# Kernel tuning notes

Hardware: AMD Instinct MI355X
Metric: run time of the kernel (lower is better)

Reference implementation:

```python
import jax, jax.numpy as jnp
import numpy as np

B, N, D = 16, 1024, 768
H = 12
HD = D // H           # 64
NUM_BUCKETS = 49      # iRPE 'product' buckets, shared across heads
SCALE = HD ** -0.5


def setup_inputs() -> dict:
    key = jax.random.key(0)
    k1, k2, k3, k4, k5, k6 = jax.random.split(key, 6)
    x = jax.random.normal(k1, (B, N, D), dtype=jnp.float32)
    qkv_w = jax.random.normal(k2, (3 * D, D), dtype=jnp.float32) * 0.02
    rpe_table = jax.random.normal(k3, (NUM_BUCKETS, HD), dtype=jnp.float32) * 0.02
    rp_bucket = jax.random.randint(k4, (N, N), 0, NUM_BUCKETS, dtype=jnp.int32)
    proj_w = jax.random.normal(k5, (D, D), dtype=jnp.float32) * 0.02
    proj_b = jax.random.normal(k6, (D,), dtype=jnp.float32) * 0.02
    return {"x": x, "qkv_w": qkv_w, "rpe_table": rpe_table,
            "rp_bucket": rp_bucket, "proj_w": proj_w, "proj_b": proj_b}


def reference(x, qkv_w, rpe_table, rp_bucket, proj_w, proj_b):
    b, n, d = x.shape
    # qkv projection (no bias), split into q,k,v of shape [B,H,N,HD]
    qkv = (x @ qkv_w.T).reshape(b, n, 3, H, HD)
    qkv = jnp.transpose(qkv, (2, 0, 3, 1, 4))
    q, k, v = qkv[0], qkv[1], qkv[2]
    q = q * SCALE
    # full attention scores [B,H,N,N]
    attn = jnp.einsum('bhid,bhjd->bhij', q, k)
    # iRPE contextual bias on keys: project q onto the bucket table, then
    # gather per relative-position bucket: bias[b,h,i,j] = (q @ W^T)[b,h,i,rp_bucket[i,j]]
    bias_all = jnp.einsum('bhid,cd->bhic', q, rpe_table)   # [B,H,N,num_buckets]
    bias = bias_all[:, :, jnp.arange(n)[:, None], rp_bucket]  # [B,H,N,N]
    attn = jax.nn.softmax(attn + bias, axis=-1)
    out = jnp.einsum('bhij,bhjd->bhid', attn, v)            # [B,H,N,HD]
    out = jnp.transpose(out, (0, 2, 1, 3)).reshape(b, n, d)
    return out @ proj_w.T + proj_b
```

## Files before the change

### kernel.cpp

```cpp
#include <hip/hip_runtime.h>

typedef short bf16x8 __attribute__((ext_vector_type(8)));
typedef float f32x4 __attribute__((ext_vector_type(4)));


__device__ __forceinline__ unsigned short f2bf(float f){
  unsigned u = __float_as_uint(f);
  u = (u + 0x7fffu + ((u >> 16) & 1u)) >> 16;
  return (unsigned short)u;
}
__device__ __forceinline__ float bf2f(unsigned short u){
  return __uint_as_float(((unsigned)u) << 16);
}
__device__ __forceinline__ f32x4 mfma16(bf16x8 a, bf16x8 b, f32x4 c){
  return __builtin_amdgcn_mfma_f32_16x16x32_bf16(a, b, c, 0, 0, 0);
}
__device__ __forceinline__ void gload_lds16(const void* g, void* l){
  __builtin_amdgcn_global_load_lds((__attribute__((address_space(1))) void*)(g),
                                   (__attribute__((address_space(3))) void*)(l), 16, 0, 0);
}

__global__ __launch_bounds__(256) void prep_kernel(
    const float* __restrict__ x, const float* __restrict__ qw,
    const float* __restrict__ pw, const int* __restrict__ rp,
    unsigned short* __restrict__ xb, unsigned short* __restrict__ wb,
    unsigned short* __restrict__ pwb, unsigned char* __restrict__ rp8){
  const int T1 = 3145728;
  const int T2 = T1 + 442368;
  const int T3 = T2 + 147456;
  const int T4 = T3 + 262144;
  for (int t = blockIdx.x * 256 + threadIdx.x; t < T4; t += gridDim.x * 256){
    if (t < T3){
      const float4* src; ushort4* dst; int off;
      if (t < T1){ src = (const float4*)x;  dst = (ushort4*)xb;  off = t; }
      else if (t < T2){ src = (const float4*)qw; dst = (ushort4*)wb;  off = t - T1; }
      else { src = (const float4*)pw; dst = (ushort4*)pwb; off = t - T2; }
      float4 v = src[off];
      ushort4 u;
      u.x = f2bf(v.x); u.y = f2bf(v.y); u.z = f2bf(v.z); u.w = f2bf(v.w);
      dst[off] = u;
    } else {
      int off = t - T3;
      int4 v = ((const int4*)rp)[off];
      uchar4 u;
      u.x = (unsigned char)v.x; u.y = (unsigned char)v.y;
      u.z = (unsigned char)v.z; u.w = (unsigned char)v.w;
      ((uchar4*)rp8)[off] = u;
    }
  }
}

__device__ __forceinline__ void gemm_core(
    const unsigned short* __restrict__ A, const unsigned short* __restrict__ Bm,
    int m0, int n0, int K, unsigned short* As, unsigned short* Bs,
    f32x4 (&acc)[4][4]){
  const int tid = threadIdx.x, lane = tid & 63, wave = tid >> 6;
  const int g = lane >> 4, r16 = lane & 15;
  const int wr = wave >> 1, wc = wave & 1;
  for (int k0 = 0; k0 < K; k0 += 32){
    __syncthreads();
    #pragma unroll
    for (int j = 0; j < 2; j++){
      int ci = j * 256 + tid;
      int row = ci >> 2, c = ci & 3;
      gload_lds16(A  + (size_t)(m0 + row) * K + k0 + c * 8,
                  (char*)As + (j * 256 + wave * 64) * 16);
      gload_lds16(Bm + (size_t)(n0 + row) * K + k0 + c * 8,
                  (char*)Bs + (j * 256 + wave * 64) * 16);
    }
    __syncthreads();
    bf16x8 a[4], b[4];
    #pragma unroll
    for (int mi = 0; mi < 4; mi++)
      a[mi] = *(const bf16x8*)((const char*)As + (wr * 64 + mi * 16 + r16) * 64 + g * 16);
    #pragma unroll
    for (int ni = 0; ni < 4; ni++)
      b[ni] = *(const bf16x8*)((const char*)Bs + (wc * 64 + ni * 16 + r16) * 64 + g * 16);
    #pragma unroll
    for (int mi = 0; mi < 4; mi++)
      #pragma unroll
      for (int ni = 0; ni < 4; ni++)
        acc[mi][ni] = mfma16(a[mi], b[ni], acc[mi][ni]);
  }
}

__global__ __launch_bounds__(256) void qkv_gemm(
    const unsigned short* __restrict__ xb, const unsigned short* __restrict__ wb,
    unsigned short* __restrict__ q_s, unsigned short* __restrict__ k_s,
    unsigned short* __restrict__ v_t){
  __shared__ __align__(16) unsigned short As[128 * 32];
  __shared__ __align__(16) unsigned short Bs[128 * 32];
  f32x4 acc[4][4];
  #pragma unroll
  for (int i = 0; i < 4; i++)
    #pragma unroll
    for (int j = 0; j < 4; j++){
      acc[i][j][0] = 0.f; acc[i][j][1] = 0.f; acc[i][j][2] = 0.f; acc[i][j][3] = 0.f;
    }
  const int m0 = blockIdx.y * 128, n0 = blockIdx.x * 128;
  gemm_core(xb, wb, m0, n0, 768, As, Bs, acc);

  const int lane = threadIdx.x & 63, wave = threadIdx.x >> 6;
  const int g = lane >> 4, r16 = lane & 15;
  const int wr = wave >> 1, wc = wave & 1;
  #pragma unroll
  for (int mi = 0; mi < 4; mi++){
    #pragma unroll
    for (int ni = 0; ni < 4; ni++){
      int gcol = n0 + wc * 64 + ni * 16 + r16;
      int sel = gcol / 768;
      int rem = gcol - sel * 768;
      int h = rem >> 6, hd = rem & 63;
      #pragma unroll
      for (int r = 0; r < 4; r++){
        int grow = m0 + wr * 64 + mi * 16 + 4 * g + r;
        int bb = grow >> 10, ii = grow & 1023;
        size_t base = ((size_t)(bb * 12 + h)) << 16;
        float v = acc[mi][ni][r];
        if (sel == 0)      q_s[base + ((size_t)ii << 6) + hd] = f2bf(v * 0.125f);
        else if (sel == 1) k_s[base + ((size_t)ii << 6) + hd] = f2bf(v);
        else               v_t[base + ((size_t)hd << 10) + ii] = f2bf(v);
      }
    }
  }
}

__global__ __launch_bounds__(256) void attn_kernel(
    const unsigned short* __restrict__ q_s, const unsigned short* __restrict__ k_s,
    const unsigned short* __restrict__ v_t, const unsigned char* __restrict__ rp8,
    const float* __restrict__ rpe, unsigned short* __restrict__ ao){
  __shared__ __align__(16) char smem[40960];
  const int tid = threadIdx.x, lane = tid & 63, w = tid >> 6;
  const int g = lane >> 4, r16 = lane & 15;
  const int qb = blockIdx.x, bh = blockIdx.y;
  const size_t bh_base = (size_t)bh << 16;

  const int i_loc = w * 16 + r16;
  const size_t qoff = bh_base + ((size_t)(qb * 64 + i_loc) << 6);
  bf16x8 qf0 = *(const bf16x8*)(q_s + qoff + g * 8);
  bf16x8 qf1 = *(const bf16x8*)(q_s + qoff + 32 + g * 8);

  float* bias_lds = (float*)(smem + 24576);
  const int s4 = (i_loc & 7) << 2;
  #pragma unroll
  for (int jt = 0; jt < 4; jt++){
    int row = jt * 16 + r16;
    bf16x8 a0, a1;
    #pragma unroll
    for (int e = 0; e < 8; e++){ a0[e] = 0; a1[e] = 0; }
    if (row < 49){
      const float* rr = rpe + row * 64 + g * 8;
      float4 x0 = *(const float4*)(rr);
      float4 x1 = *(const float4*)(rr + 4);
      float4 y0 = *(const float4*)(rr + 32);
      float4 y1 = *(const float4*)(rr + 36);
      a0[0]=f2bf(x0.x); a0[1]=f2bf(x0.y); a0[2]=f2bf(x0.z); a0[3]=f2bf(x0.w);
      a0[4]=f2bf(x1.x); a0[5]=f2bf(x1.y); a0[6]=f2bf(x1.z); a0[7]=f2bf(x1.w);
      a1[0]=f2bf(y0.x); a1[1]=f2bf(y0.y); a1[2]=f2bf(y0.z); a1[3]=f2bf(y0.w);
      a1[4]=f2bf(y1.x); a1[5]=f2bf(y1.y); a1[6]=f2bf(y1.z); a1[7]=f2bf(y1.w);
    }
    f32x4 z = {0.f, 0.f, 0.f, 0.f};
    z = mfma16(a0, qf0, z);
    z = mfma16(a1, qf1, z);
    *(f32x4*)(bias_lds + i_loc * 64 + ((jt * 16 + 4 * g) ^ s4)) = z;
  }

  unsigned short* ks = (unsigned short*)smem;
  unsigned short* vs = (unsigned short*)(smem + 8192);
  char* pbuf = smem + 16384 + w * 2048;
  const unsigned char* rprow = rp8 + ((size_t)(qb * 64 + i_loc) << 10);
  const float* brow = bias_lds + i_loc * 64;

  f32x4 o[4];
  #pragma unroll
  for (int dt = 0; dt < 4; dt++){ o[dt][0]=0.f; o[dt][1]=0.f; o[dt][2]=0.f; o[dt][3]=0.f; }
  float m_i = -INFINITY, l_i = 0.f;

  for (int kb = 0; kb < 16; kb++){
    __syncthreads();
    #pragma unroll
    for (int j = 0; j < 2; j++){
      int ci = j * 256 + tid;
      int row = ci >> 3, c = ci & 7;
      int sc = c ^ (row & 7);
      gload_lds16(k_s + bh_base + ((size_t)(kb * 64 + row) << 6) + sc * 8,
                  (char*)smem + (j * 256 + w * 64) * 16);
      gload_lds16(v_t + bh_base + ((size_t)row << 10) + kb * 64 + sc * 8,
                  (char*)smem + 8192 + (j * 256 + w * 64) * 16);
    }
    __syncthreads();

    f32x4 st[4];
    #pragma unroll
    for (int jt = 0; jt < 4; jt++){
      int krow = jt * 16 + r16;
      int sw = (krow & 7) << 4;
      bf16x8 ka0 = *(const bf16x8*)((char*)ks + krow * 128 + ((g * 16) ^ sw));
      bf16x8 ka1 = *(const bf16x8*)((char*)ks + krow * 128 + ((64 + g * 16) ^ sw));
      f32x4 z = {0.f, 0.f, 0.f, 0.f};
      z = mfma16(ka0, qf0, z);
      z = mfma16(ka1, qf1, z);
      st[jt] = z;
    }
    #pragma unroll
    for (int jt = 0; jt < 4; jt++){
      uchar4 bu = *(const uchar4*)(rprow + kb * 64 + jt * 16 + g * 4);
      st[jt][0] += brow[bu.x ^ s4];
      st[jt][1] += brow[bu.y ^ s4];
      st[jt][2] += brow[bu.z ^ s4];
      st[jt][3] += brow[bu.w ^ s4];
    }
    float tmax = -INFINITY;
    #pragma unroll
    for (int jt = 0; jt < 4; jt++)
      tmax = fmaxf(tmax, fmaxf(fmaxf(st[jt][0], st[jt][1]), fmaxf(st[jt][2], st[jt][3])));
    tmax = fmaxf(tmax, __shfl_xor(tmax, 16));
    tmax = fmaxf(tmax, __shfl_xor(tmax, 32));
    float mnew = fmaxf(m_i, tmax);
    float alpha = __expf(m_i - mnew);
    float psum = 0.f;
    #pragma unroll
    for (int jt = 0; jt < 4; jt++){
      float p0 = __expf(st[jt][0] - mnew);
      float p1 = __expf(st[jt][1] - mnew);
      float p2 = __expf(st[jt][2] - mnew);
      float p3 = __expf(st[jt][3] - mnew);
      psum += p0 + p1 + p2 + p3;
      ushort4 u; u.x = f2bf(p0); u.y = f2bf(p1); u.z = f2bf(p2); u.w = f2bf(p3);
      *(ushort4*)(pbuf + r16 * 128 + ((jt * 32 + g * 8) ^ ((r16 & 7) << 4))) = u;
    }
    psum += __shfl_xor(psum, 16);
    psum += __shfl_xor(psum, 32);
    l_i = l_i * alpha + psum;
    m_i = mnew;
    float af[4];
    #pragma unroll
    for (int r = 0; r < 4; r++) af[r] = __shfl(alpha, 4 * g + r);
    #pragma unroll
    for (int dt = 0; dt < 4; dt++){
      o[dt][0] *= af[0]; o[dt][1] *= af[1]; o[dt][2] *= af[2]; o[dt][3] *= af[3];
    }
    #pragma unroll
    for (int kt = 0; kt < 2; kt++){
      bf16x8 pa = *(const bf16x8*)(pbuf + r16 * 128 + ((kt * 64 + g * 16) ^ ((r16 & 7) << 4)));
      #pragma unroll
      for (int dt = 0; dt < 4; dt++){
        int vrow = dt * 16 + r16;
        bf16x8 vb = *(const bf16x8*)((char*)vs + vrow * 128 + ((kt * 64 + g * 16) ^ ((vrow & 7) << 4)));
        o[dt] = mfma16(pa, vb, o[dt]);
      }
    }
  }

  float lf[4];
  #pragma unroll
  for (int r = 0; r < 4; r++) lf[r] = 1.f / __shfl(l_i, 4 * g + r);
  const int bidx = bh / 12, h = bh - bidx * 12;
  #pragma unroll
  for (int dt = 0; dt < 4; dt++){
    int d = dt * 16 + r16;
    #pragma unroll
    for (int r = 0; r < 4; r++){
      int i = qb * 64 + w * 16 + 4 * g + r;
      ao[(size_t)(bidx * 1024 + i) * 768 + h * 64 + d] = f2bf(o[dt][r] * lf[r]);
    }
  }
}

__global__ __launch_bounds__(256) void proj_gemm(
    const unsigned short* __restrict__ aob, const unsigned short* __restrict__ pwb,
    const float* __restrict__ pb, float* __restrict__ out){
  __shared__ __align__(16) unsigned short As[128 * 32];
  __shared__ __align__(16) unsigned short Bs[128 * 32];
  f32x4 acc[4][4];
  #pragma unroll
  for (int i = 0; i < 4; i++)
    #pragma unroll
    for (int j = 0; j < 4; j++){
      acc[i][j][0] = 0.f; acc[i][j][1] = 0.f; acc[i][j][2] = 0.f; acc[i][j][3] = 0.f;
    }
  const int m0 = blockIdx.y * 128, n0 = blockIdx.x * 128;
  gemm_core(aob, pwb, m0, n0, 768, As, Bs, acc);

  const int lane = threadIdx.x & 63, wave = threadIdx.x >> 6;
  const int g = lane >> 4, r16 = lane & 15;
  const int wr = wave >> 1, wc = wave & 1;
  #pragma unroll
  for (int mi = 0; mi < 4; mi++){
    #pragma unroll
    for (int ni = 0; ni < 4; ni++){
      int gcol = n0 + wc * 64 + ni * 16 + r16;
      float bias = pb[gcol];
      #pragma unroll
      for (int r = 0; r < 4; r++){
        int grow = m0 + wr * 64 + mi * 16 + 4 * g + r;
        out[(size_t)grow * 768 + gcol] = acc[mi][ni][r] + bias;
      }
    }
  }
}

extern "C" void kernel_launch(void* const* d_in, const int* in_sizes, int n_in,
                              void* d_out, int out_size, void* d_ws, size_t ws_size,
                              hipStream_t stream){
  const float* x      = (const float*)d_in[0];
  const float* qkv_w  = (const float*)d_in[1];
  const float* rpe    = (const float*)d_in[2];
  const int*   rp     = (const int*)d_in[3];
  const float* proj_w = (const float*)d_in[4];
  const float* proj_b = (const float*)d_in[5];
  float* out = (float*)d_out;
  char* ws = (char*)d_ws;

  unsigned short* xb  = (unsigned short*)(ws);
  unsigned short* wb  = (unsigned short*)(ws + 25165824);
  unsigned short* pwb = (unsigned short*)(ws + 28704768);
  unsigned char*  rp8 = (unsigned char*) (ws + 29884416);
  unsigned short* q_s = (unsigned short*)(ws + 30932992);
  unsigned short* k_s = (unsigned short*)(ws + 56098816);
  unsigned short* v_t = (unsigned short*)(ws + 81264640);
  unsigned short* aob = (unsigned short*)(ws + 106430464);

  prep_kernel<<<2048, 256, 0, stream>>>(x, qkv_w, proj_w, rp, xb, wb, pwb, rp8);
  qkv_gemm<<<dim3(18, 128), 256, 0, stream>>>(xb, wb, q_s, k_s, v_t);
  attn_kernel<<<dim3(16, 192), 256, 0, stream>>>(q_s, k_s, v_t, rp8, rpe, aob);
  proj_gemm<<<dim3(6, 128), 256, 0, stream>>>(aob, pwb, proj_b, out);
}
```

Before: 342.2 us.

## Fold log2e into Q scale, use exp2, lazy rescale, precomputed bias offsets

The Q scale now includes log2(e) so softmax can use the raw v_exp_f32 (exp2) instruction. The running-max rescale of O and l is skipped when the new tile max stays within 8 of the old max. Bucket indices are pre-multiplied by 4 and pre-XOR-swizzled in the prep kernel, so the bias lookup becomes a direct byte offset. The kernel also hoists K/V load address computation out of the loop and packs bf16 conversion with v_cvt_pk_bf16_f32. Lazy rescaling lets exponentials reach up to 2^8 before renormalisation, which trades a little precision headroom for fewer multiplies and shuffles.

```diff
diff --git a/kernel.cpp b/kernel.cpp
--- a/kernel.cpp
+++ b/kernel.cpp
@@ -3,21 +3,29 @@
 typedef short bf16x8 __attribute__((ext_vector_type(8)));
 typedef float f32x4 __attribute__((ext_vector_type(4)));
 
+#define QSCALE 0.1803368801111204f
 
 __device__ __forceinline__ unsigned short f2bf(float f){
   unsigned u = __float_as_uint(f);
   u = (u + 0x7fffu + ((u >> 16) & 1u)) >> 16;
   return (unsigned short)u;
 }
-__device__ __forceinline__ float bf2f(unsigned short u){
-  return __uint_as_float(((unsigned)u) << 16);
-}
 __device__ __forceinline__ f32x4 mfma16(bf16x8 a, bf16x8 b, f32x4 c){
   return __builtin_amdgcn_mfma_f32_16x16x32_bf16(a, b, c, 0, 0, 0);
 }
 __device__ __forceinline__ void gload_lds16(const void* g, void* l){
   __builtin_amdgcn_global_load_lds((__attribute__((address_space(1))) void*)(g),
                                    (__attribute__((address_space(3))) void*)(l), 16, 0, 0);
+}
+__device__ __forceinline__ unsigned cvt_pk_bf16(float lo, float hi){
+  unsigned r;
+  asm("v_cvt_pk_bf16_f32 %0, %1, %2" : "=v"(r) : "v"(lo), "v"(hi));
+  return r;
+}
+__device__ __forceinline__ float exp2_fast(float x){
+  float r;
+  asm("v_exp_f32 %0, %1" : "=v"(r) : "v"(x));
+  return r;
 }
 
 __global__ __launch_bounds__(256) void prep_kernel(
@@ -42,9 +50,13 @@
     } else {
       int off = t - T3;
       int4 v = ((const int4*)rp)[off];
+      int row = (off * 4) >> 10;
+      int sw = (row & 7) << 4;
       uchar4 u;
-      u.x = (unsigned char)v.x; u.y = (unsigned char)v.y;
-      u.z = (unsigned char)v.z; u.w = (unsigned char)v.w;
+      u.x = (unsigned char)((v.x << 2) ^ sw);
+      u.y = (unsigned char)((v.y << 2) ^ sw);
+      u.z = (unsigned char)((v.z << 2) ^ sw);
+      u.w = (unsigned char)((v.w << 2) ^ sw);
       ((uchar4*)rp8)[off] = u;
     }
   }
@@ -117,7 +129,7 @@
         int bb = grow >> 10, ii = grow & 1023;
         size_t base = ((size_t)(bb * 12 + h)) << 16;
         float v = acc[mi][ni][r];
-        if (sel == 0)      q_s[base + ((size_t)ii << 6) + hd] = f2bf(v * 0.125f);
+        if (sel == 0)      q_s[base + ((size_t)ii << 6) + hd] = f2bf(v * QSCALE);
         else if (sel == 1) k_s[base + ((size_t)ii << 6) + hd] = f2bf(v);
         else               v_t[base + ((size_t)hd << 10) + ii] = f2bf(v);
       }
@@ -168,8 +180,20 @@
   unsigned short* ks = (unsigned short*)smem;
   unsigned short* vs = (unsigned short*)(smem + 8192);
   char* pbuf = smem + 16384 + w * 2048;
+  const char* browb = (const char*)bias_lds + i_loc * 256;
+
+  const int ci0 = tid, ci1 = 256 + tid;
+  const int row0 = ci0 >> 3, sc0 = (ci0 & 7) ^ (row0 & 7);
+  const int row1 = ci1 >> 3, sc1 = (ci1 & 7) ^ (row1 & 7);
+  const char* kp0 = (const char*)(k_s + bh_base) + row0 * 128 + sc0 * 16;
+  const char* kp1 = (const char*)(k_s + bh_base) + row1 * 128 + sc1 * 16;
+  const char* vp0 = (const char*)(v_t + bh_base) + row0 * 2048 + sc0 * 16;
+  const char* vp1 = (const char*)(v_t + bh_base) + row1 * 2048 + sc1 * 16;
+  char* kl0 = (char*)smem + w * 1024;
+  char* kl1 = (char*)smem + 4096 + w * 1024;
+  char* vl0 = (char*)smem + 8192 + w * 1024;
+  char* vl1 = (char*)smem + 12288 + w * 1024;
   const unsigned char* rprow = rp8 + ((size_t)(qb * 64 + i_loc) << 10);
-  const float* brow = bias_lds + i_loc * 64;
 
   f32x4 o[4];
   #pragma unroll
@@ -178,16 +202,11 @@
 
   for (int kb = 0; kb < 16; kb++){
     __syncthreads();
-    #pragma unroll
-    for (int j = 0; j < 2; j++){
-      int ci = j * 256 + tid;
-      int row = ci >> 3, c = ci & 7;
-      int sc = c ^ (row & 7);
-      gload_lds16(k_s + bh_base + ((size_t)(kb * 64 + row) << 6) + sc * 8,
-                  (char*)smem + (j * 256 + w * 64) * 16);
-      gload_lds16(v_t + bh_base + ((size_t)row << 10) + kb * 64 + sc * 8,
-                  (char*)smem + 8192 + (j * 256 + w * 64) * 16);
-    }
+    gload_lds16(kp0, kl0);
+    gload_lds16(kp1, kl1);
+    gload_lds16(vp0, vl0);
+    gload_lds16(vp1, vl1);
+    kp0 += 8192; kp1 += 8192; vp0 += 128; vp1 += 128;
     __syncthreads();
 
     f32x4 st[4];
@@ -204,11 +223,11 @@
     }
     #pragma unroll
     for (int jt = 0; jt < 4; jt++){
-      uchar4 bu = *(const uchar4*)(rprow + kb * 64 + jt * 16 + g * 4);
-      st[jt][0] += brow[bu.x ^ s4];
-      st[jt][1] += brow[bu.y ^ s4];
-      st[jt][2] += brow[bu.z ^ s4];
-      st[jt][3] += brow[bu.w ^ s4];
+      unsigned bu = *(const unsigned*)(rprow + kb * 64 + jt * 16 + g * 4);
+      st[jt][0] += *(const float*)(browb + (bu & 0xff));
+      st[jt][1] += *(const float*)(browb + ((bu >> 8) & 0xff));
+      st[jt][2] += *(const float*)(browb + ((bu >> 16) & 0xff));
+      st[jt][3] += *(const float*)(browb + (bu >> 24));
     }
     float tmax = -INFINITY;
     #pragma unroll
@@ -216,30 +235,38 @@
       tmax = fmaxf(tmax, fmaxf(fmaxf(st[jt][0], st[jt][1]), fmaxf(st[jt][2], st[jt][3])));
     tmax = fmaxf(tmax, __shfl_xor(tmax, 16));
     tmax = fmaxf(tmax, __shfl_xor(tmax, 32));
-    float mnew = fmaxf(m_i, tmax);
-    float alpha = __expf(m_i - mnew);
+    const bool skip = __all(tmax <= m_i + 8.f);
+    float mnew = m_i, alpha;
+    if (!skip){
+      mnew = fmaxf(m_i, tmax);
+      alpha = exp2_fast(m_i - mnew);
+    }
     float psum = 0.f;
     #pragma unroll
     for (int jt = 0; jt < 4; jt++){
-      float p0 = __expf(st[jt][0] - mnew);
-      float p1 = __expf(st[jt][1] - mnew);
-      float p2 = __expf(st[jt][2] - mnew);
-      float p3 = __expf(st[jt][3] - mnew);
-      psum += p0 + p1 + p2 + p3;
-      ushort4 u; u.x = f2bf(p0); u.y = f2bf(p1); u.z = f2bf(p2); u.w = f2bf(p3);
-      *(ushort4*)(pbuf + r16 * 128 + ((jt * 32 + g * 8) ^ ((r16 & 7) << 4))) = u;
+      float p0 = exp2_fast(st[jt][0] - mnew);
+      float p1 = exp2_fast(st[jt][1] - mnew);
+      float p2 = exp2_fast(st[jt][2] - mnew);
+      float p3 = exp2_fast(st[jt][3] - mnew);
+      psum += (p0 + p1) + (p2 + p3);
+      uint2 u; u.x = cvt_pk_bf16(p0, p1); u.y = cvt_pk_bf16(p2, p3);
+      *(uint2*)(pbuf + r16 * 128 + ((jt * 32 + g * 8) ^ ((r16 & 7) << 4))) = u;
     }
     psum += __shfl_xor(psum, 16);
     psum += __shfl_xor(psum, 32);
-    l_i = l_i * alpha + psum;
+    if (!skip){
+      l_i = l_i * alpha + psum;
+      float af[4];
+      #pragma unroll
+      for (int r = 0; r < 4; r++) af[r] = __shfl(alpha, 4 * g + r);
+      #pragma unroll
+      for (int dt = 0; dt < 4; dt++){
+        o[dt][0] *= af[0]; o[dt][1] *= af[1]; o[dt][2] *= af[2]; o[dt][3] *= af[3];
+      }
+    } else {
+      l_i += psum;
+    }
     m_i = mnew;
-    float af[4];
-    #pragma unroll
-    for (int r = 0; r < 4; r++) af[r] = __shfl(alpha, 4 * g + r);
-    #pragma unroll
-    for (int dt = 0; dt < 4; dt++){
-      o[dt][0] *= af[0]; o[dt][1] *= af[1]; o[dt][2] *= af[2]; o[dt][3] *= af[3];
-    }
     #pragma unroll
     for (int kt = 0; kt < 2; kt++){
       bf16x8 pa = *(const bf16x8*)(pbuf + r16 * 128 + ((kt * 64 + g * 16) ^ ((r16 & 7) << 4)));
```

After: 309.3 us. 9.6% less time.
